# Optimization experiments

Measured on AMD Instinct MI355X. Metric: run time of the kernel, lower is better.

## Reference

```python
import jax, jax.numpy as jnp
import numpy as np

N = 100000      # nodes
E = 1600000     # edges per node-kind graph
H = 2           # attention heads
F_IN = 64
F_OUT = 64
N_USER = 90000
D2 = 64
NB_CLASSES = 2


def setup_inputs() -> dict:
    key = jax.random.key(0)
    ks = jax.random.split(key, 16)
    xav = lambda k, shape: jax.random.normal(k, shape, jnp.float32) * np.sqrt(2.0 / (shape[-2] + shape[-1]))
    inp = {
        "h": jax.random.normal(ks[0], (N, F_IN), jnp.float32),
        "src0": jax.random.randint(ks[1], (E,), 0, N, jnp.int32),
        "trg0": jax.random.randint(ks[2], (E,), 0, N, jnp.int32),
        "src1": jax.random.randint(ks[3], (E,), 0, N, jnp.int32),
        "trg1": jax.random.randint(ks[4], (E,), 0, N, jnp.int32),
        # SpGATLayer params per node kind
        "w0": xav(ks[5], (H, F_IN, F_OUT)),
        "asrc0": xav(ks[6], (H, F_OUT)),   # attn_src squeezed from (H, F_OUT, 1)
        "atrg0": xav(ks[7], (H, F_OUT)),
        "w1": xav(ks[8], (H, F_IN, F_OUT)),
        "asrc1": xav(ks[9], (H, F_OUT)),
        "atrg1": xav(ks[10], (H, F_OUT)),
        # AdditiveAttention params (nn.Linear weights: [out, in])
        "aa_w1": xav(ks[11], (D2, F_IN)),
        "aa_w2": xav(ks[12], (D2, F_OUT)),
        "aa_m": xav(ks[13], (1, D2)),
        # final fc: in = d1 * (nb_node_kinds + 1) = 64 * 3
        "fc_w": xav(ks[14], (NB_CLASSES, F_OUT * 3)),
        "fc_b": jnp.zeros((NB_CLASSES,), jnp.float32),
        "n_user": N_USER,
    }
    return inp


def sp_gat_layer(h, w, a_src, a_trg, src, trg, n):
    # h: [N, F_IN]; w: [H, F_IN, F_OUT]
    hp = jnp.einsum("nf,hfo->hno", h, w)                  # [H, N, F_OUT]
    attn_src = jnp.einsum("hno,ho->nh", hp, a_src)        # [N, H]
    attn_trg = jnp.einsum("hno,ho->nh", hp, a_trg)        # [N, H]
    e = jax.nn.leaky_relu(attn_src[src] + attn_trg[trg], 0.2)  # [E, H]
    e = e - jnp.max(e)                                    # global max, as in source
    exp_e = jnp.exp(e)
    denom = jax.ops.segment_sum(exp_e, trg, num_segments=n)[trg] + 1e-16
    attn = (exp_e / denom)[:, :, None]                    # [E, H, 1]
    hp_nhf = jnp.transpose(hp, (1, 0, 2))                 # [N, H, F_OUT]
    h_weighted = hp_nhf[src] * attn                       # [E, H, F_OUT]
    out = jax.ops.segment_sum(h_weighted, trg, num_segments=n)  # [N, H, F_OUT]
    return out


def reference(h, src0, trg0, src1, trg1, w0, asrc0, atrg0, w1, asrc1, atrg1,
              aa_w1, aa_w2, aa_m, fc_w, fc_b, n_user):
    n = h.shape[0]
    # one SpGAT layer per node kind, then mean over heads (final-layer branch)
    x0 = sp_gat_layer(h, w0, asrc0, atrg0, src0, trg0, n).mean(axis=1)  # [N, F_OUT]
    x1 = sp_gat_layer(h, w1, asrc1, atrg1, src1, trg1, n).mean(axis=1)
    type_aware = jnp.stack([x0[:n_user], x1[:n_user]], axis=1)          # [n_user, 2, F_OUT]
    # AdditiveAttention
    feat = h[:n_user]                                                   # [n_user, F_IN]
    q = jnp.tanh(feat @ aa_w1.T[:, None, :].squeeze(1)[None][0] if False else
                 jnp.tanh(0.0))  # placeholder removed below
    q = jnp.tanh(feat[:, None, :] @ aa_w1.T + type_aware @ aa_w2.T)     # [n_user, 2, D2]
    scores = (q @ aa_m.T).squeeze(-1)                                   # [n_user, 2]
    beta = jax.nn.softmax(scores, axis=-1)
    type_fusion = jnp.einsum("nk,nkd->nd", beta, type_aware)[:, None, :]  # [n_user, 1, F_OUT]
    cat = jnp.concatenate([type_aware, type_fusion], axis=1).reshape(n_user, -1)  # [n_user, 3*F_OUT]
    logits = cat @ fc_w.T + fc_b
    return jax.nn.log_softmax(logits, axis=-1)
```

## Files before the change

kernel.cpp:

```cpp
#include <hip/hip_runtime.h>
#include <hip/hip_bf16.h>
#include <math.h>

#define N_NODES 100000
#define N_EDGES 1600000
#define N_USER  90000
#define NBUCK   256
#define BSZ     352
#define TILE    2048

typedef __attribute__((ext_vector_type(8))) short  short8;
typedef __attribute__((ext_vector_type(4))) float  floatx4;
typedef unsigned int  uint;
typedef unsigned short ushort;

__device__ __forceinline__ ushort f2bf(float x) {
  uint u = __float_as_uint(x);
  u += 0x7fffu + ((u >> 16) & 1u);
  return (ushort)(u >> 16);
}
__device__ __forceinline__ float bf2f(ushort v) { return __uint_as_float(((uint)v) << 16); }

__device__ __forceinline__ void split8(const float v[8], short8& hi, short8& lo) {
  #pragma unroll
  for (int j = 0; j < 8; ++j) {
    ushort h = f2bf(v[j]);
    hi[j] = (short)h;
    lo[j] = (short)f2bf(v[j] - bf2f(h));
  }
}
__device__ __forceinline__ void load_split8(const float* p, short8& hi, short8& lo) {
  const float4* q = (const float4*)p;
  float4 a = q[0], b = q[1];
  float v[8] = {a.x, a.y, a.z, a.w, b.x, b.y, b.z, b.w};
  split8(v, hi, lo);
}
__device__ __forceinline__ float fast_tanh(float x) {
  float t = __expf(2.f * x);
  return 1.f - 2.f / (t + 1.f);
}

__global__ __launch_bounds__(256) void hp_mfma(
    const float* __restrict__ h, const float* __restrict__ w,
    const float* __restrict__ a_src, const float* __restrict__ a_trg,
    uint* __restrict__ hpi, float* __restrict__ attn_src, float* __restrict__ attn_trg)
{
  __shared__ float part[4][16][4];
  const int tid = threadIdx.x, lane = tid & 63, wv = tid >> 6;
  const int quad = lane >> 4, l15 = lane & 15;
  const int o = wv * 16 + l15;
  const float vas0 = a_src[o], vas1 = a_src[64 + o];
  const float vat0 = a_trg[o], vat1 = a_trg[64 + o];
  short8 b0h[2], b0l[2], b1h[2], b1l[2];
  #pragma unroll
  for (int ks = 0; ks < 2; ++ks) {
    float v0[8], v1[8];
    #pragma unroll
    for (int j = 0; j < 8; ++j) {
      int k = quad * 8 + j + ks * 32;
      v0[j] = w[k * 64 + o];
      v1[j] = w[4096 + k * 64 + o];
    }
    split8(v0, b0h[ks], b0l[ks]);
    split8(v1, b1h[ks], b1l[ks]);
  }
  for (int t = blockIdx.x; t < N_NODES / 16; t += gridDim.x) {
    int m0 = t * 16, arow = m0 + l15;
    short8 ah[2], al[2];
    #pragma unroll
    for (int ks = 0; ks < 2; ++ks)
      load_split8(h + arow * 64 + quad * 8 + ks * 32, ah[ks], al[ks]);
    floatx4 c0 = {0.f, 0.f, 0.f, 0.f}, c1 = {0.f, 0.f, 0.f, 0.f};
    #pragma unroll
    for (int ks = 0; ks < 2; ++ks) {
      c0 = __builtin_amdgcn_mfma_f32_16x16x32_bf16(ah[ks], b0h[ks], c0, 0, 0, 0);
      c0 = __builtin_amdgcn_mfma_f32_16x16x32_bf16(ah[ks], b0l[ks], c0, 0, 0, 0);
      c0 = __builtin_amdgcn_mfma_f32_16x16x32_bf16(al[ks], b0h[ks], c0, 0, 0, 0);
      c1 = __builtin_amdgcn_mfma_f32_16x16x32_bf16(ah[ks], b1h[ks], c1, 0, 0, 0);
      c1 = __builtin_amdgcn_mfma_f32_16x16x32_bf16(ah[ks], b1l[ks], c1, 0, 0, 0);
      c1 = __builtin_amdgcn_mfma_f32_16x16x32_bf16(al[ks], b1h[ks], c1, 0, 0, 0);
    }
    #pragma unroll
    for (int r = 0; r < 4; ++r) {
      int n = m0 + quad * 4 + r;
      hpi[n * 64 + o] = (uint)f2bf(c0[r]) | ((uint)f2bf(c1[r]) << 16);
    }
    #pragma unroll
    for (int r = 0; r < 4; ++r) {
      float pas0 = c0[r] * vas0, pas1 = c1[r] * vas1;
      float pat0 = c0[r] * vat0, pat1 = c1[r] * vat1;
      #pragma unroll
      for (int m = 1; m < 16; m <<= 1) {
        pas0 += __shfl_xor(pas0, m, 64); pas1 += __shfl_xor(pas1, m, 64);
        pat0 += __shfl_xor(pat0, m, 64); pat1 += __shfl_xor(pat1, m, 64);
      }
      if (l15 == 0) {
        part[wv][quad * 4 + r][0] = pas0; part[wv][quad * 4 + r][1] = pas1;
        part[wv][quad * 4 + r][2] = pat0; part[wv][quad * 4 + r][3] = pat1;
      }
    }
    __syncthreads();
    if (tid < 64) {
      int row = tid & 15, which = tid >> 4;
      float v = part[0][row][which] + part[1][row][which]
              + part[2][row][which] + part[3][row][which];
      int n = m0 + row;
      if (which == 0)      attn_src[n * 2]     = v;
      else if (which == 1) attn_src[n * 2 + 1] = v;
      else if (which == 2) attn_trg[n * 2]     = v;
      else                 attn_trg[n * 2 + 1] = v;
    }
    __syncthreads();
  }
}

__global__ __launch_bounds__(256) void bhist_kernel(const int* __restrict__ trg, int* __restrict__ bhist)
{
  __shared__ int hh[NBUCK];
  hh[threadIdx.x] = 0;
  __syncthreads();
  const int base = blockIdx.x * TILE;
  #pragma unroll
  for (int j = 0; j < 8; ++j) {
    int e = base + j * 256 + threadIdx.x;
    if (e < N_EDGES) {
      int t = trg[e];
      if (t < N_USER) atomicAdd(&hh[t / BSZ], 1);
    }
  }
  __syncthreads();
  if (hh[threadIdx.x]) atomicAdd(&bhist[threadIdx.x], hh[threadIdx.x]);
}

__global__ __launch_bounds__(256) void scanb_kernel(const int* __restrict__ bhist,
                                                    int* __restrict__ bstart, int* __restrict__ bcur)
{
  __shared__ int s[256];
  int v = bhist[threadIdx.x];
  s[threadIdx.x] = v;
  __syncthreads();
  for (int d = 1; d < 256; d <<= 1) {
    int t = (threadIdx.x >= d) ? s[threadIdx.x - d] : 0;
    __syncthreads();
    s[threadIdx.x] += t;
    __syncthreads();
  }
  int excl = s[threadIdx.x] - v;
  bstart[threadIdx.x] = excl;
  bcur[threadIdx.x * 16] = excl;
  if (threadIdx.x == 255) bstart[256] = s[255];
}

__global__ __launch_bounds__(256) void bucket_kernel(
    const int* __restrict__ src, const int* __restrict__ trg,
    int* __restrict__ bcur, uint2* __restrict__ pairbuf)
{
  __shared__ uint2 plds[TILE];
  __shared__ int bcnt[NBUCK], bscan[NBUCK], gbase[NBUCK];
  const int tid = threadIdx.x;
  const int base = blockIdx.x * TILE;
  bcnt[tid] = 0;
  __syncthreads();
  int myb[8], myr[8];
  uint2 myp[8];
  #pragma unroll
  for (int j = 0; j < 8; ++j) {
    int e = base + j * 256 + tid;
    myb[j] = -1;
    if (e < N_EDGES) {
      int t = trg[e];
      if (t < N_USER) {
        int b = t / BSZ;
        myb[j] = b;
        myr[j] = atomicAdd(&bcnt[b], 1);
        myp[j].x = (uint)src[e];
        myp[j].y = (uint)t;
      }
    }
  }
  __syncthreads();
  gbase[tid] = atomicAdd(&bcur[tid * 16], bcnt[tid]);
  bscan[tid] = bcnt[tid];
  __syncthreads();
  for (int d = 1; d < 256; d <<= 1) {
    int v = (tid >= d) ? bscan[tid - d] : 0;
    __syncthreads();
    bscan[tid] += v;
    __syncthreads();
  }
  #pragma unroll
  for (int j = 0; j < 8; ++j)
    if (myb[j] >= 0) plds[bscan[myb[j]] - bcnt[myb[j]] + myr[j]] = myp[j];
  __syncthreads();
  int total = bscan[NBUCK - 1];
  for (int i = tid; i < total; i += 256) {
    uint2 pr = plds[i];
    int b = (int)pr.y / BSZ;
    int idx = gbase[b] + (i - (bscan[b] - bcnt[b]));
    if (idx >= 0 && idx < N_EDGES) pairbuf[idx] = pr;
  }
}

__global__ __launch_bounds__(256) void fine_kernel(
    const uint2* __restrict__ pairbuf, const int* __restrict__ bstart,
    int* __restrict__ offs, int* __restrict__ csr_src,
    const float* __restrict__ attn_src, const float* __restrict__ attn_trg,
    float2* __restrict__ wgt)
{
  __shared__ int cnt[BSZ + 1];
  __shared__ int cur[BSZ];
  const int b = blockIdx.x, tid = threadIdx.x;
  const int t0 = b * BSZ;
  const int nt = min(BSZ, N_USER - t0);
  const int pbeg = bstart[b], pend = bstart[b + 1];
  for (int j = tid; j <= BSZ; j += 256) cnt[j] = 0;
  __syncthreads();
  for (int i = pbeg + tid; i < pend; i += 256) {
    int tl = (int)pairbuf[i].y - t0;
    tl = min(max(tl, 0), BSZ - 1);
    atomicAdd(&cnt[tl], 1);
  }
  __syncthreads();
  if (tid == 0) {
    int run = 0;
    for (int j = 0; j < nt; ++j) { int c = cnt[j]; cnt[j] = run; run += c; }
    cnt[nt] = run;
  }
  __syncthreads();
  for (int j = tid; j < nt; j += 256) {
    offs[t0 + j] = pbeg + cnt[j];
    cur[j] = cnt[j];
  }
  if (tid == 0 && t0 + nt == N_USER) offs[N_USER] = pbeg + cnt[nt];
  __syncthreads();
  const float2* as2 = (const float2*)attn_src;
  const float2* at2 = (const float2*)attn_trg;
  for (int i = pbeg + tid; i < pend; i += 256) {
    uint2 pr = pairbuf[i];
    int s = min((int)pr.x, N_NODES - 1);
    int tt = min((int)pr.y, N_USER - 1);
    int tl = min(max(tt - t0, 0), BSZ - 1);
    float2 as = as2[s];
    float2 at = at2[tt];
    float e0 = as.x + at.x; e0 = (e0 > 0.f) ? e0 : 0.2f * e0;
    float e1 = as.y + at.y; e1 = (e1 > 0.f) ? e1 : 0.2f * e1;
    int p = pbeg + atomicAdd(&cur[tl], 1);
    p = min(max(p, 0), N_EDGES - 1);
    csr_src[p] = s;
    wgt[p] = make_float2(__expf(e0), __expf(e1));
  }
}

__global__ __launch_bounds__(256) void accum_kernel(
    const int* __restrict__ offs, const int* __restrict__ csr_src,
    const float2* __restrict__ wgt,
    const uint* __restrict__ hpi, float* __restrict__ x)
{
  const int lane = threadIdx.x & 63, wv = threadIdx.x >> 6;
  int n = blockIdx.x * 4 + wv;
  if (n >= N_USER) return;
  int beg = max(0, offs[n]);
  int end = min(offs[n + 1], N_EDGES);
  int deg = end - beg;
  float acc0 = 0.f, acc1 = 0.f, den0 = 0.f, den1 = 0.f;
  for (int base = 0; base < deg; base += 64) {
    int rem = min(64, deg - base);
    int sv = 0;
    if (lane < rem) sv = csr_src[beg + base + lane];
    int j = 0;
    for (; j + 8 <= rem; j += 8) {
      int ss[8]; uint pv[8]; float2 W[8];
      #pragma unroll
      for (int u = 0; u < 8; ++u) ss[u] = __shfl(sv, j + u, 64);
      #pragma unroll
      for (int u = 0; u < 8; ++u) {
        int s = min(max(ss[u], 0), N_NODES - 1);
        pv[u] = hpi[s * 64 + lane];
      }
      #pragma unroll
      for (int u = 0; u < 8; ++u) W[u] = wgt[beg + base + j + u];
      #pragma unroll
      for (int u = 0; u < 8; ++u) {
        den0 += W[u].x; den1 += W[u].y;
        acc0 += W[u].x * bf2f((ushort)(pv[u] & 0xffffu));
        acc1 += W[u].y * bf2f((ushort)(pv[u] >> 16));
      }
    }
    for (; j < rem; ++j) {
      int s = min(max(__shfl(sv, j, 64), 0), N_NODES - 1);
      uint pv = hpi[s * 64 + lane];
      float2 W = wgt[beg + base + j];
      den0 += W.x; den1 += W.y;
      acc0 += W.x * bf2f((ushort)(pv & 0xffffu));
      acc1 += W.y * bf2f((ushort)(pv >> 16));
    }
  }
  x[n * 64 + lane] = 0.5f * (acc0 / (den0 + 1e-16f) + acc1 / (den1 + 1e-16f));
}

__global__ __launch_bounds__(256) void final_mfma(
    const float* __restrict__ h, const float* __restrict__ x0, const float* __restrict__ x1,
    const float* __restrict__ aa_w1, const float* __restrict__ aa_w2, const float* __restrict__ aa_m,
    const float* __restrict__ fc_w, const float* __restrict__ fc_b, float* __restrict__ out)
{
  __shared__ float aam_s[64], fcw_s[384], fcb_s[2];
  __shared__ float scw0[4][16], scw1[4][16];
  const int tid = threadIdx.x;
  if (tid < 64)  aam_s[tid] = aa_m[tid];
  for (int i = tid; i < 384; i += 256) fcw_s[i] = fc_w[i];
  if (tid < 2)   fcb_s[tid] = fc_b[tid];
  const int lane = tid & 63, wv = tid >> 6, quad = lane >> 4, l15 = lane & 15;
  const int d = wv * 16 + l15;
  short8 b1h[2], b1l[2], b2h[2], b2l[2];
  #pragma unroll
  for (int ks = 0; ks < 2; ++ks) {
    load_split8(aa_w1 + d * 64 + quad * 8 + ks * 32, b1h[ks], b1l[ks]);
    load_split8(aa_w2 + d * 64 + quad * 8 + ks * 32, b2h[ks], b2l[ks]);
  }
  __syncthreads();
  for (int t = blockIdx.x; t < N_USER / 16; t += gridDim.x) {
    int m0 = t * 16, arow = m0 + l15;
    const int erow = m0 + wv * 4 + quad;
    float4 ev0 = *(const float4*)(x0 + erow * 64 + l15 * 4);
    float4 ev1 = *(const float4*)(x1 + erow * 64 + l15 * 4);
    short8 ahh[2], ahl[2], a0h[2], a0l[2], a1h[2], a1l[2];
    #pragma unroll
    for (int ks = 0; ks < 2; ++ks) {
      load_split8(h  + arow * 64 + quad * 8 + ks * 32, ahh[ks], ahl[ks]);
      load_split8(x0 + arow * 64 + quad * 8 + ks * 32, a0h[ks], a0l[ks]);
      load_split8(x1 + arow * 64 + quad * 8 + ks * 32, a1h[ks], a1l[ks]);
    }
    floatx4 t1a = {0.f,0.f,0.f,0.f}, t20a = {0.f,0.f,0.f,0.f}, t21a = {0.f,0.f,0.f,0.f};
    #pragma unroll
    for (int ks = 0; ks < 2; ++ks) {
      t1a  = __builtin_amdgcn_mfma_f32_16x16x32_bf16(ahh[ks], b1h[ks], t1a, 0, 0, 0);
      t1a  = __builtin_amdgcn_mfma_f32_16x16x32_bf16(ahh[ks], b1l[ks], t1a, 0, 0, 0);
      t1a  = __builtin_amdgcn_mfma_f32_16x16x32_bf16(ahl[ks], b1h[ks], t1a, 0, 0, 0);
      t20a = __builtin_amdgcn_mfma_f32_16x16x32_bf16(a0h[ks], b2h[ks], t20a, 0, 0, 0);
      t20a = __builtin_amdgcn_mfma_f32_16x16x32_bf16(a0h[ks], b2l[ks], t20a, 0, 0, 0);
      t20a = __builtin_amdgcn_mfma_f32_16x16x32_bf16(a0l[ks], b2h[ks], t20a, 0, 0, 0);
      t21a = __builtin_amdgcn_mfma_f32_16x16x32_bf16(a1h[ks], b2h[ks], t21a, 0, 0, 0);
      t21a = __builtin_amdgcn_mfma_f32_16x16x32_bf16(a1h[ks], b2l[ks], t21a, 0, 0, 0);
      t21a = __builtin_amdgcn_mfma_f32_16x16x32_bf16(a1l[ks], b2h[ks], t21a, 0, 0, 0);
    }
    float am = aam_s[d];
    #pragma unroll
    for (int r = 0; r < 4; ++r) {
      float q0 = fast_tanh(t1a[r] + t20a[r]);
      float q1 = fast_tanh(t1a[r] + t21a[r]);
      float p0 = q0 * am, p1 = q1 * am;
      #pragma unroll
      for (int m = 1; m < 16; m <<= 1) { p0 += __shfl_xor(p0, m, 64); p1 += __shfl_xor(p1, m, 64); }
      if (l15 == 0) { scw0[wv][quad * 4 + r] = p0; scw1[wv][quad * 4 + r] = p1; }
    }
    __syncthreads();
    {
      int row = wv * 4 + quad, n = m0 + row;
      float s0 = scw0[0][row] + scw0[1][row] + scw0[2][row] + scw0[3][row];
      float s1 = scw1[0][row] + scw1[1][row] + scw1[2][row] + scw1[3][row];
      float mx = fmaxf(s0, s1);
      float e0 = __expf(s0 - mx), e1 = __expf(s1 - mx);
      float inv = 1.f / (e0 + e1);
      float b0 = e0 * inv, b1 = e1 * inv;
      float a0[4] = {ev0.x, ev0.y, ev0.z, ev0.w};
      float a1[4] = {ev1.x, ev1.y, ev1.z, ev1.w};
      float pc0 = 0.f, pc1 = 0.f;
      #pragma unroll
      for (int c = 0; c < 4; ++c) {
        int o = l15 * 4 + c;
        float fv = b0 * a0[c] + b1 * a1[c];
        pc0 += fcw_s[o] * a0[c] + fcw_s[64 + o] * a1[c] + fcw_s[128 + o] * fv;
        pc1 += fcw_s[192 + o] * a0[c] + fcw_s[256 + o] * a1[c] + fcw_s[320 + o] * fv;
      }
      #pragma unroll
      for (int m = 1; m < 16; m <<= 1) { pc0 += __shfl_xor(pc0, m, 64); pc1 += __shfl_xor(pc1, m, 64); }
      if (l15 == 0) {
        float l0 = pc0 + fcb_s[0], l1 = pc1 + fcb_s[1];
        float lm = fmaxf(l0, l1);
        float lse = lm + logf(__expf(l0 - lm) + __expf(l1 - lm));
        out[n * 2] = l0 - lse;
        out[n * 2 + 1] = l1 - lse;
      }
    }
    __syncthreads();
  }
}

extern "C" void kernel_launch(void* const* d_in, const int* in_sizes, int n_in,
                              void* d_out, int out_size, void* d_ws, size_t ws_size,
                              hipStream_t stream)
{
  const float* h     = (const float*)d_in[0];
  const int*   src0  = (const int*)d_in[1];
  const int*   trg0  = (const int*)d_in[2];
  const int*   src1  = (const int*)d_in[3];
  const int*   trg1  = (const int*)d_in[4];
  const float* w0    = (const float*)d_in[5];
  const float* asrc0 = (const float*)d_in[6];
  const float* atrg0 = (const float*)d_in[7];
  const float* w1    = (const float*)d_in[8];
  const float* asrc1 = (const float*)d_in[9];
  const float* atrg1 = (const float*)d_in[10];
  const float* aa_w1 = (const float*)d_in[11];
  const float* aa_w2 = (const float*)d_in[12];
  const float* aa_m  = (const float*)d_in[13];
  const float* fc_w  = (const float*)d_in[14];
  const float* fc_b  = (const float*)d_in[15];
  float* out = (float*)d_out;

  char* ws = (char*)d_ws;
  size_t off = 0;
  auto alloc = [&](size_t bytes) -> void* {
    void* p = ws + off;
    off = (off + bytes + 255) & ~(size_t)255;
    return p;
  };
  uint*   hpi      = (uint*)alloc((size_t)N_NODES * 64 * 4);
  float*  attn_src = (float*)alloc((size_t)N_NODES * 2 * 4);
  float*  attn_trg = (float*)alloc((size_t)N_NODES * 2 * 4);
  float*  x0       = (float*)alloc((size_t)N_USER * 64 * 4);
  float*  x1       = (float*)alloc((size_t)N_USER * 64 * 4);
  int*    offs     = (int*)alloc((size_t)(N_USER + 1) * 4);
  int*    csr      = (int*)alloc((size_t)N_EDGES * 4);
  uint2*  pairbuf  = (uint2*)alloc((size_t)N_EDGES * 8);
  float2* wgt      = (float2*)alloc((size_t)N_EDGES * 8);
  int*    bhist    = (int*)alloc((size_t)NBUCK * 4);
  int*    bstart   = (int*)alloc((size_t)(NBUCK + 1) * 4);
  int*    bcur     = (int*)alloc((size_t)NBUCK * 16 * 4);

  const int TB = (N_EDGES + TILE - 1) / TILE;
  for (int layer = 0; layer < 2; ++layer) {
    const float* w    = layer ? w1 : w0;
    const float* asrc = layer ? asrc1 : asrc0;
    const float* atrg = layer ? atrg1 : atrg0;
    const int*   src  = layer ? src1 : src0;
    const int*   trg  = layer ? trg1 : trg0;
    float*       x    = layer ? x1 : x0;
    hipLaunchKernelGGL(hp_mfma, dim3(1024), dim3(256), 0, stream,
                       h, w, asrc, atrg, hpi, attn_src, attn_trg);
    hipMemsetAsync(bhist, 0, (size_t)NBUCK * 4, stream);
    hipLaunchKernelGGL(bhist_kernel, dim3(TB), dim3(256), 0, stream, trg, bhist);
    hipLaunchKernelGGL(scanb_kernel, dim3(1), dim3(256), 0, stream, bhist, bstart, bcur);
    hipLaunchKernelGGL(bucket_kernel, dim3(TB), dim3(256), 0, stream, src, trg, bcur, pairbuf);
    hipLaunchKernelGGL(fine_kernel, dim3(NBUCK), dim3(256), 0, stream,
                       pairbuf, bstart, offs, csr, attn_src, attn_trg, wgt);
    hipLaunchKernelGGL(accum_kernel, dim3(N_USER / 4), dim3(256), 0, stream,
                       offs, csr, wgt, hpi, x);
  }
  hipLaunchKernelGGL(final_mfma, dim3(5625), dim3(256), 0, stream,
                     h, x0, x1, aa_w1, aa_w2, aa_m, fc_w, fc_b, out);
}
```

Baseline: 499.2 us.

## Batch both GAT layers into single merged kernel launches per stage

```diff
diff --git a/kernel.cpp b/kernel.cpp
--- a/kernel.cpp
+++ b/kernel.cpp
@@ -8,6 +8,9 @@
 #define NBUCK   256
 #define BSZ     352
 #define TILE    2048
+#define TBLK    782
+#define ACCB    22500
+#define HPB     1024
 
 typedef __attribute__((ext_vector_type(8))) short  short8;
 typedef __attribute__((ext_vector_type(4))) float  floatx4;
@@ -40,11 +43,24 @@
   return 1.f - 2.f / (t + 1.f);
 }
 
-__global__ __launch_bounds__(256) void hp_mfma(
-    const float* __restrict__ h, const float* __restrict__ w,
-    const float* __restrict__ a_src, const float* __restrict__ a_trg,
-    uint* __restrict__ hpi, float* __restrict__ attn_src, float* __restrict__ attn_trg)
-{
+__global__ __launch_bounds__(256) void hp_mfma2(
+    const float* __restrict__ h,
+    const float* __restrict__ wA,  const float* __restrict__ wB,
+    const float* __restrict__ asA, const float* __restrict__ asB,
+    const float* __restrict__ atA, const float* __restrict__ atB,
+    uint* __restrict__ hpiA, uint* __restrict__ hpiB,
+    float* __restrict__ attnsA, float* __restrict__ attnsB,
+    float* __restrict__ attntA, float* __restrict__ attntB, int base)
+{
+  const int layer = (blockIdx.x >= base) ? 1 : 0;
+  const int bid = blockIdx.x - layer * base;
+  const float* w     = layer ? wB : wA;
+  const float* a_src = layer ? asB : asA;
+  const float* a_trg = layer ? atB : atA;
+  uint*  hpi      = layer ? hpiB : hpiA;
+  float* attn_src = layer ? attnsB : attnsA;
+  float* attn_trg = layer ? attntB : attntA;
+
   __shared__ float part[4][16][4];
   const int tid = threadIdx.x, lane = tid & 63, wv = tid >> 6;
   const int quad = lane >> 4, l15 = lane & 15;
@@ -64,7 +80,7 @@
     split8(v0, b0h[ks], b0l[ks]);
     split8(v1, b1h[ks], b1l[ks]);
   }
-  for (int t = blockIdx.x; t < N_NODES / 16; t += gridDim.x) {
+  for (int t = bid; t < N_NODES / 16; t += base) {
     int m0 = t * 16, arow = m0 + l15;
     short8 ah[2], al[2];
     #pragma unroll
@@ -114,29 +130,39 @@
   }
 }
 
-__global__ __launch_bounds__(256) void bhist_kernel(const int* __restrict__ trg, int* __restrict__ bhist)
-{
+__global__ __launch_bounds__(256) void bhist2(
+    const int* __restrict__ trgA, const int* __restrict__ trgB,
+    int* __restrict__ bhist, int base)
+{
+  const int layer = (blockIdx.x >= base) ? 1 : 0;
+  const int bid = blockIdx.x - layer * base;
+  const int* trg = layer ? trgB : trgA;
+  int* bh = bhist + layer * NBUCK;
   __shared__ int hh[NBUCK];
   hh[threadIdx.x] = 0;
   __syncthreads();
-  const int base = blockIdx.x * TILE;
+  const int b0 = bid * TILE;
   #pragma unroll
   for (int j = 0; j < 8; ++j) {
-    int e = base + j * 256 + threadIdx.x;
+    int e = b0 + j * 256 + threadIdx.x;
     if (e < N_EDGES) {
       int t = trg[e];
       if (t < N_USER) atomicAdd(&hh[t / BSZ], 1);
     }
   }
   __syncthreads();
-  if (hh[threadIdx.x]) atomicAdd(&bhist[threadIdx.x], hh[threadIdx.x]);
-}
-
-__global__ __launch_bounds__(256) void scanb_kernel(const int* __restrict__ bhist,
-                                                    int* __restrict__ bstart, int* __restrict__ bcur)
-{
+  if (hh[threadIdx.x]) atomicAdd(&bh[threadIdx.x], hh[threadIdx.x]);
+}
+
+__global__ __launch_bounds__(256) void scanb2(const int* __restrict__ bhist,
+                                              int* __restrict__ bstart, int* __restrict__ bcur)
+{
+  const int layer = blockIdx.x;
+  const int* bh = bhist + layer * NBUCK;
+  int* bs = bstart + layer * (NBUCK + 1);
+  int* bc = bcur + layer * NBUCK * 16;
   __shared__ int s[256];
-  int v = bhist[threadIdx.x];
+  int v = bh[threadIdx.x];
   s[threadIdx.x] = v;
   __syncthreads();
   for (int d = 1; d < 256; d <<= 1) {
@@ -146,26 +172,34 @@
     __syncthreads();
   }
   int excl = s[threadIdx.x] - v;
-  bstart[threadIdx.x] = excl;
-  bcur[threadIdx.x * 16] = excl;
-  if (threadIdx.x == 255) bstart[256] = s[255];
-}
-
-__global__ __launch_bounds__(256) void bucket_kernel(
-    const int* __restrict__ src, const int* __restrict__ trg,
-    int* __restrict__ bcur, uint2* __restrict__ pairbuf)
-{
+  bs[threadIdx.x] = excl;
+  bc[threadIdx.x * 16] = excl;
+  if (threadIdx.x == 255) bs[256] = s[255];
+}
+
+__global__ __launch_bounds__(256) void bucket2(
+    const int* __restrict__ srcA, const int* __restrict__ srcB,
+    const int* __restrict__ trgA, const int* __restrict__ trgB,
+    int* __restrict__ bcur, uint2* __restrict__ pairbufA, uint2* __restrict__ pairbufB, int base)
+{
+  const int layer = (blockIdx.x >= base) ? 1 : 0;
+  const int bid = blockIdx.x - layer * base;
+  const int* src = layer ? srcB : srcA;
+  const int* trg = layer ? trgB : trgA;
+  int* bc = bcur + layer * NBUCK * 16;
+  uint2* pairbuf = layer ? pairbufB : pairbufA;
+
   __shared__ uint2 plds[TILE];
   __shared__ int bcnt[NBUCK], bscan[NBUCK], gbase[NBUCK];
   const int tid = threadIdx.x;
-  const int base = blockIdx.x * TILE;
+  const int b0 = bid * TILE;
   bcnt[tid] = 0;
   __syncthreads();
   int myb[8], myr[8];
   uint2 myp[8];
   #pragma unroll
   for (int j = 0; j < 8; ++j) {
-    int e = base + j * 256 + tid;
+    int e = b0 + j * 256 + tid;
     myb[j] = -1;
     if (e < N_EDGES) {
       int t = trg[e];
@@ -179,7 +213,7 @@
     }
   }
   __syncthreads();
-  gbase[tid] = atomicAdd(&bcur[tid * 16], bcnt[tid]);
+  gbase[tid] = atomicAdd(&bc[tid * 16], bcnt[tid]);
   bscan[tid] = bcnt[tid];
   __syncthreads();
   for (int d = 1; d < 256; d <<= 1) {
@@ -201,18 +235,31 @@
   }
 }
 
-__global__ __launch_bounds__(256) void fine_kernel(
-    const uint2* __restrict__ pairbuf, const int* __restrict__ bstart,
-    int* __restrict__ offs, int* __restrict__ csr_src,
-    const float* __restrict__ attn_src, const float* __restrict__ attn_trg,
-    float2* __restrict__ wgt)
-{
+__global__ __launch_bounds__(256) void fine2(
+    const uint2* __restrict__ pairbufA, const uint2* __restrict__ pairbufB,
+    const int* __restrict__ bstart,
+    int* __restrict__ offsA, int* __restrict__ offsB,
+    int* __restrict__ csrA,  int* __restrict__ csrB,
+    const float* __restrict__ attnsA, const float* __restrict__ attnsB,
+    const float* __restrict__ attntA, const float* __restrict__ attntB,
+    float2* __restrict__ wgtA, float2* __restrict__ wgtB, int base)
+{
+  const int layer = (blockIdx.x >= base) ? 1 : 0;
+  const int b = blockIdx.x - layer * base;
+  const uint2* pairbuf = layer ? pairbufB : pairbufA;
+  const int* bs = bstart + layer * (NBUCK + 1);
+  int* offs = layer ? offsB : offsA;
+  int* csr_src = layer ? csrB : csrA;
+  const float* attn_src = layer ? attnsB : attnsA;
+  const float* attn_trg = layer ? attntB : attntA;
+  float2* wgt = layer ? wgtB : wgtA;
+
   __shared__ int cnt[BSZ + 1];
   __shared__ int cur[BSZ];
-  const int b = blockIdx.x, tid = threadIdx.x;
+  const int tid = threadIdx.x;
   const int t0 = b * BSZ;
   const int nt = min(BSZ, N_USER - t0);
-  const int pbeg = bstart[b], pend = bstart[b + 1];
+  const int pbeg = bs[b], pend = bs[b + 1];
   for (int j = tid; j <= BSZ; j += 256) cnt[j] = 0;
   __syncthreads();
   for (int i = pbeg + tid; i < pend; i += 256) {
@@ -251,22 +298,32 @@
   }
 }
 
-__global__ __launch_bounds__(256) void accum_kernel(
-    const int* __restrict__ offs, const int* __restrict__ csr_src,
-    const float2* __restrict__ wgt,
-    const uint* __restrict__ hpi, float* __restrict__ x)
-{
+__global__ __launch_bounds__(256) void accum2(
+    const int* __restrict__ offsA, const int* __restrict__ offsB,
+    const int* __restrict__ csrA,  const int* __restrict__ csrB,
+    const float2* __restrict__ wgtA, const float2* __restrict__ wgtB,
+    const uint* __restrict__ hpiA, const uint* __restrict__ hpiB,
+    float* __restrict__ xA, float* __restrict__ xB, int base)
+{
+  const int layer = (blockIdx.x >= base) ? 1 : 0;
+  const int bid = blockIdx.x - layer * base;
+  const int* offs = layer ? offsB : offsA;
+  const int* csr_src = layer ? csrB : csrA;
+  const float2* wgt = layer ? wgtB : wgtA;
+  const uint* hpi = layer ? hpiB : hpiA;
+  float* x = layer ? xB : xA;
+
   const int lane = threadIdx.x & 63, wv = threadIdx.x >> 6;
-  int n = blockIdx.x * 4 + wv;
+  int n = bid * 4 + wv;
   if (n >= N_USER) return;
   int beg = max(0, offs[n]);
   int end = min(offs[n + 1], N_EDGES);
   int deg = end - beg;
   float acc0 = 0.f, acc1 = 0.f, den0 = 0.f, den1 = 0.f;
-  for (int base = 0; base < deg; base += 64) {
-    int rem = min(64, deg - base);
+  for (int base2 = 0; base2 < deg; base2 += 64) {
+    int rem = min(64, deg - base2);
     int sv = 0;
-    if (lane < rem) sv = csr_src[beg + base + lane];
+    if (lane < rem) sv = csr_src[beg + base2 + lane];
     int j = 0;
     for (; j + 8 <= rem; j += 8) {
       int ss[8]; uint pv[8]; float2 W[8];
@@ -278,7 +335,7 @@
         pv[u] = hpi[s * 64 + lane];
       }
       #pragma unroll
-      for (int u = 0; u < 8; ++u) W[u] = wgt[beg + base + j + u];
+      for (int u = 0; u < 8; ++u) W[u] = wgt[beg + base2 + j + u];
       #pragma unroll
       for (int u = 0; u < 8; ++u) {
         den0 += W[u].x; den1 += W[u].y;
@@ -289,7 +346,7 @@
     for (; j < rem; ++j) {
       int s = min(max(__shfl(sv, j, 64), 0), N_NODES - 1);
       uint pv = hpi[s * 64 + lane];
-      float2 W = wgt[beg + base + j];
+      float2 W = wgt[beg + base2 + j];
       den0 += W.x; den1 += W.y;
       acc0 += W.x * bf2f((ushort)(pv & 0xffffu));
       acc1 += W.y * bf2f((ushort)(pv >> 16));
@@ -408,6 +465,9 @@
   const float* fc_b  = (const float*)d_in[15];
   float* out = (float*)d_out;
 
+  const int nl = (ws_size >= (size_t)172 * 1024 * 1024) ? 2 : 1;
+  const size_t L = (size_t)(nl - 1);
+
   char* ws = (char*)d_ws;
   size_t off = 0;
   auto alloc = [&](size_t bytes) -> void* {
@@ -415,38 +475,64 @@
     off = (off + bytes + 255) & ~(size_t)255;
     return p;
   };
-  uint*   hpi      = (uint*)alloc((size_t)N_NODES * 64 * 4);
-  float*  attn_src = (float*)alloc((size_t)N_NODES * 2 * 4);
-  float*  attn_trg = (float*)alloc((size_t)N_NODES * 2 * 4);
+  uint*   hpi      = (uint*)alloc((size_t)nl * N_NODES * 64 * 4);
+  float*  attn_src = (float*)alloc((size_t)nl * N_NODES * 2 * 4);
+  float*  attn_trg = (float*)alloc((size_t)nl * N_NODES * 2 * 4);
   float*  x0       = (float*)alloc((size_t)N_USER * 64 * 4);
   float*  x1       = (float*)alloc((size_t)N_USER * 64 * 4);
-  int*    offs     = (int*)alloc((size_t)(N_USER + 1) * 4);
-  int*    csr      = (int*)alloc((size_t)N_EDGES * 4);
-  uint2*  pairbuf  = (uint2*)alloc((size_t)N_EDGES * 8);
-  float2* wgt      = (float2*)alloc((size_t)N_EDGES * 8);
-  int*    bhist    = (int*)alloc((size_t)NBUCK * 4);
-  int*    bstart   = (int*)alloc((size_t)(NBUCK + 1) * 4);
-  int*    bcur     = (int*)alloc((size_t)NBUCK * 16 * 4);
-
-  const int TB = (N_EDGES + TILE - 1) / TILE;
-  for (int layer = 0; layer < 2; ++layer) {
-    const float* w    = layer ? w1 : w0;
-    const float* asrc = layer ? asrc1 : asrc0;
-    const float* atrg = layer ? atrg1 : atrg0;
-    const int*   src  = layer ? src1 : src0;
-    const int*   trg  = layer ? trg1 : trg0;
-    float*       x    = layer ? x1 : x0;
-    hipLaunchKernelGGL(hp_mfma, dim3(1024), dim3(256), 0, stream,
-                       h, w, asrc, atrg, hpi, attn_src, attn_trg);
-    hipMemsetAsync(bhist, 0, (size_t)NBUCK * 4, stream);
-    hipLaunchKernelGGL(bhist_kernel, dim3(TB), dim3(256), 0, stream, trg, bhist);
-    hipLaunchKernelGGL(scanb_kernel, dim3(1), dim3(256), 0, stream, bhist, bstart, bcur);
-    hipLaunchKernelGGL(bucket_kernel, dim3(TB), dim3(256), 0, stream, src, trg, bcur, pairbuf);
-    hipLaunchKernelGGL(fine_kernel, dim3(NBUCK), dim3(256), 0, stream,
-                       pairbuf, bstart, offs, csr, attn_src, attn_trg, wgt);
-    hipLaunchKernelGGL(accum_kernel, dim3(N_USER / 4), dim3(256), 0, stream,
-                       offs, csr, wgt, hpi, x);
-  }
-  hipLaunchKernelGGL(final_mfma, dim3(5625), dim3(256), 0, stream,
+  int*    offs     = (int*)alloc((size_t)nl * (N_USER + 1) * 4);
+  int*    csr      = (int*)alloc((size_t)nl * N_EDGES * 4);
+  uint2*  pairbuf  = (uint2*)alloc((size_t)nl * N_EDGES * 8);
+  float2* wgt      = (float2*)alloc((size_t)nl * N_EDGES * 8);
+  int*    bhist    = (int*)alloc((size_t)2 * NBUCK * 4);
+  int*    bstart   = (int*)alloc((size_t)2 * (NBUCK + 1) * 4);
+  int*    bcur     = (int*)alloc((size_t)2 * NBUCK * 16 * 4);
+
+  uint*   hpi1     = hpi + L * (size_t)N_NODES * 64;
+  float*  attns1   = attn_src + L * (size_t)N_NODES * 2;
+  float*  attnt1   = attn_trg + L * (size_t)N_NODES * 2;
+  int*    offs1    = offs + L * (size_t)(N_USER + 1);
+  int*    csr1     = csr + L * (size_t)N_EDGES;
+  uint2*  pairbuf1 = pairbuf + L * (size_t)N_EDGES;
+  float2* wgt1     = wgt + L * (size_t)N_EDGES;
+
+  if (nl == 2) {
+    hipLaunchKernelGGL(hp_mfma2, dim3(2 * HPB), dim3(256), 0, stream,
+                       h, w0, w1, asrc0, asrc1, atrg0, atrg1,
+                       hpi, hpi1, attn_src, attns1, attn_trg, attnt1, HPB);
+    hipMemsetAsync(bhist, 0, (size_t)2 * NBUCK * 4, stream);
+    hipLaunchKernelGGL(bhist2, dim3(2 * TBLK), dim3(256), 0, stream, trg0, trg1, bhist, TBLK);
+    hipLaunchKernelGGL(scanb2, dim3(2), dim3(256), 0, stream, bhist, bstart, bcur);
+    hipLaunchKernelGGL(bucket2, dim3(2 * TBLK), dim3(256), 0, stream,
+                       src0, src1, trg0, trg1, bcur, pairbuf, pairbuf1, TBLK);
+    hipLaunchKernelGGL(fine2, dim3(2 * NBUCK), dim3(256), 0, stream,
+                       pairbuf, pairbuf1, bstart, offs, offs1, csr, csr1,
+                       attn_src, attns1, attn_trg, attnt1, wgt, wgt1, NBUCK);
+    hipLaunchKernelGGL(accum2, dim3(2 * ACCB), dim3(256), 0, stream,
+                       offs, offs1, csr, csr1, wgt, wgt1, hpi, hpi1, x0, x1, ACCB);
+  } else {
+    for (int layer = 0; layer < 2; ++layer) {
+      const float* w    = layer ? w1 : w0;
+      const float* asrc = layer ? asrc1 : asrc0;
+      const float* atrg = layer ? atrg1 : atrg0;
+      const int*   src  = layer ? src1 : src0;
+      const int*   trg  = layer ? trg1 : trg0;
+      float*       x    = layer ? x1 : x0;
+      hipLaunchKernelGGL(hp_mfma2, dim3(HPB), dim3(256), 0, stream,
+                         h, w, w, asrc, asrc, atrg, atrg,
+                         hpi, hpi, attn_src, attn_src, attn_trg, attn_trg, HPB);
+      hipMemsetAsync(bhist, 0, (size_t)NBUCK * 4, stream);
+      hipLaunchKernelGGL(bhist2, dim3(TBLK), dim3(256), 0, stream, trg, trg, bhist, TBLK);
+      hipLaunchKernelGGL(scanb2, dim3(1), dim3(256), 0, stream, bhist, bstart, bcur);
+      hipLaunchKernelGGL(bucket2, dim3(TBLK), dim3(256), 0, stream,
+                         src, src, trg, trg, bcur, pairbuf, pairbuf, TBLK);
+      hipLaunchKernelGGL(fine2, dim3(NBUCK), dim3(256), 0, stream,
+                         pairbuf, pairbuf, bstart, offs, offs, csr, csr,
+                         attn_src, attn_src, attn_trg, attn_trg, wgt, wgt, NBUCK);
+      hipLaunchKernelGGL(accum2, dim3(ACCB), dim3(256), 0, stream,
+                         offs, offs, csr, csr, wgt, wgt, hpi, hpi, x, x, ACCB);
+    }
+  }
+  hipLaunchKernelGGL(final_mfma, dim3(1875), dim3(256), 0, stream,
                      h, x0, x1, aa_w1, aa_w2, aa_m, fc_w, fc_b, out);
 }
```

After: 467.2 us. 6.4% less time.
